# Kernel optimization log

Hardware: AMD Instinct MI355X
Metric: run time of the kernel (lower is better)

Reference implementation:

```python
import jax, jax.numpy as jnp
from jax import lax
import numpy as np

# dims
N_ENT, M, K = 2048, 64, 32              # entities, mentions, candidates per mention
LT, LB, LM, LC, LD = 32, 128, 16, 128, 512  # char lengths: title, body, mention, context, doc
VOCAB, EMB = 5053, 300
H, HH, CCS, W = 256, 128, 512, 5        # hidden, per-dir LSTM hidden, char channels, conv width


def char_cnn(idx, emb, conv_w, conv_b):
    # Conv2d(1, CCS, [EMB, W]) applied to (N,1,EMB,L) == Conv1d(EMB, CCS, W); relu + max-pool over length
    x = jnp.swapaxes(emb[idx], 1, 2)                        # [N, EMB, L]
    y = lax.conv_general_dilated(x, conv_w, (1,), 'VALID')  # [N, CCS, L-W+1]
    return jax.nn.relu(y + conv_b[None, :, None]).max(axis=2)  # [N, CCS]


def _lstm_dir(x, Wih, Whh, bih, bhh):
    pre = x @ Wih.T + (bih + bhh)                            # [B, T, 4*HH]
    def step(carry, g_t):
        h, c = carry
        i, f, g, o = jnp.split(g_t + h @ Whh.T, 4, axis=-1)
        c = jax.nn.sigmoid(f) * c + jax.nn.sigmoid(i) * jnp.tanh(g)
        h = jax.nn.sigmoid(o) * jnp.tanh(c)
        return (h, c), h
    B = x.shape[0]
    z = jnp.zeros((B, Whh.shape[1]), x.dtype)
    _, hs = lax.scan(step, (z, z), jnp.swapaxes(pre, 0, 1))
    return jnp.swapaxes(hs, 0, 1)


def bilstm(x, Wih_f, Whh_f, bih_f, bhh_f, Wih_b, Whh_b, bih_b, bhh_b):
    fwd = _lstm_dir(x, Wih_f, Whh_f, bih_f, bhh_f)
    bwd = _lstm_dir(x[:, ::-1], Wih_b, Whh_b, bih_b, bhh_b)[:, ::-1]
    return jnp.concatenate([fwd, bwd], axis=-1)              # [B, T, H]


def att_flow(c, q, wc, bc, wq, bq, wcq, bcq):
    # BiDAF attention; c,q: [B,T,H] -> [B,T,4H]
    s = (c @ wc)[:, :, None] + (q @ wq)[:, None, :] \
        + jnp.einsum('bid,bjd,d->bij', c, q, wcq) + (bc + bq + bcq)
    a = jax.nn.softmax(s, axis=2)
    c2q = jnp.einsum('bij,bjd->bid', a, q)
    b = jax.nn.softmax(s.max(axis=2), axis=1)
    q2c = jnp.einsum('bi,bid->bd', b, c)[:, None, :]
    return jnp.concatenate([c, c2q, c * c2q, c * jnp.broadcast_to(q2c, c.shape)], axis=-1)


def setup_inputs() -> dict:
    key = jax.random.key(0)
    ks = jax.random.split(key, 16)
    rng = np.random.RandomState(0)
    # exactly K distinct candidate entities per mention (regularized mention_entity indicator)
    cand_idx = jnp.asarray(np.argsort(rng.rand(M, N_ENT), axis=1)[:, :K])
    emb = jax.random.uniform(ks[0], (VOCAB, EMB), jnp.float32, -0.001, 0.001).at[1].set(0.0)
    def rnd(k, shape, s=0.05):
        return jax.random.normal(k, shape, jnp.float32) * s
    return {
        'title_vec': jax.random.randint(ks[1], (N_ENT, LT), 0, VOCAB),
        'body_vec': jax.random.randint(ks[2], (N_ENT, LB), 0, VOCAB),
        'mention_vec': jax.random.randint(ks[3], (M, LM), 0, VOCAB),
        'context_vec': jax.random.randint(ks[4], (M, LC), 0, VOCAB),
        'doc_vec': jax.random.randint(ks[5], (LD,), 0, VOCAB),
        'cand_idx': cand_idx,
        'emb': emb,
        'conv_w': rnd(ks[6], (CCS, EMB, W), 0.02), 'conv_b': jnp.zeros((CCS,), jnp.float32),
        'Wih_f': rnd(ks[7], (4 * HH, CCS)), 'Whh_f': rnd(ks[8], (4 * HH, HH)),
        'bih_f': jnp.zeros((4 * HH,), jnp.float32), 'bhh_f': jnp.zeros((4 * HH,), jnp.float32),
        'Wih_b': rnd(ks[9], (4 * HH, CCS)), 'Whh_b': rnd(ks[10], (4 * HH, HH)),
        'bih_b': jnp.zeros((4 * HH,), jnp.float32), 'bhh_b': jnp.zeros((4 * HH,), jnp.float32),
        'wc': rnd(ks[11], (H,)), 'bc': jnp.zeros((), jnp.float32),
        'wq': rnd(ks[12], (H,)), 'bq': jnp.zeros((), jnp.float32),
        'wcq': rnd(ks[13], (H,)), 'bcq': jnp.zeros((), jnp.float32),
        'wz': rnd(ks[14], (4 * H,)), 'bz': jnp.zeros((), jnp.float32),
        'w_p1': jnp.asarray(0.7, jnp.float32), 'b_p1': jnp.asarray(0.1, jnp.float32),
        'w_p2': jnp.asarray(0.5, jnp.float32), 'b_p2': jnp.asarray(-0.1, jnp.float32),
    }


def reference(title_vec, body_vec, mention_vec, context_vec, doc_vec, cand_idx,
              emb, conv_w, conv_b,
              Wih_f, Whh_f, bih_f, bhh_f, Wih_b, Whh_b, bih_b, bhh_b,
              wc, bc, wq, bq, wcq, bcq, wz, bz, w_p1, b_p1, w_p2, b_p2):
    m, k = cand_idx.shape
    n = title_vec.shape[0]
    lstm_p = (Wih_f, Whh_f, bih_f, bhh_f, Wih_b, Whh_b, bih_b, bhh_b)
    # char-CNN features (compute once per unique sequence, then gather / broadcast)
    title_feat = char_cnn(title_vec, emb, conv_w, conv_b)         # [n, CCS]
    body_feat = char_cnn(body_vec, emb, conv_w, conv_b)           # [n, CCS]
    ctx_feat = char_cnn(context_vec, emb, conv_w, conv_b)         # [m, CCS]
    doc_feat = char_cnn(doc_vec[None], emb, conv_w, conv_b)[0]    # [CCS]
    # per-mention candidate sequences (seq dim = candidates, as in the original loop)
    title_h = bilstm(title_feat[cand_idx], *lstm_p)               # [m, k, H]
    body_h = bilstm(body_feat[cand_idx], *lstm_p)
    ctx_h = bilstm(jnp.broadcast_to(ctx_feat[:, None, :], (m, k, CCS)), *lstm_p)
    doc_h = bilstm(jnp.broadcast_to(doc_feat[None, None, :], (1, k, CCS)), *lstm_p)
    doc_h = jnp.broadcast_to(doc_h, (m, k, H))
    g = att_flow(ctx_h, title_h, wc, bc, wq, bq, wcq, bcq)        # [m, k, 4H]
    h = att_flow(doc_h, body_h, wc, bc, wq, bq, wcq, bcq)
    p1 = g @ wz + bz                                              # [m, k]
    p2 = h @ wz + bz
    score = w_p1 * p1 + b_p1 + w_p2 * p2 + b_p2
    # len(true_output)==1 branch is always taken in the original: raw scores, softmax, sum-normalized
    score_sm = jax.nn.softmax(score, axis=1)
    score_un = score / score.sum(axis=1, keepdims=True)
    rows = jnp.arange(m)[:, None]
    def scatter(v):
        return jnp.zeros((m, n), v.dtype).at[rows, cand_idx].set(v)
    return scatter(score), scatter(score_sm), scatter(score_un)
```

## Files before the change

kernel.cpp:

```cpp
#include <hip/hip_runtime.h>
#include <hip/hip_fp16.h>
#include <math.h>

#define DEDUP_B 34439168ULL
#define AH_B    34459648ULL
#define BH_B    37695488ULL
#define BHP_B   39333888ULL
#define WHH_B   40382464ULL
#define AHP_B   34459648ULL

typedef _Float16 half8 __attribute__((ext_vector_type(8)));
typedef float f32x4 __attribute__((ext_vector_type(4)));

__device__ inline void add8(float* a, float4 r){
  const __half2* h = (const __half2*)&r;
  #pragma unroll
  for (int q = 0; q < 4; ++q){
    float2 f = __half22float2(h[q]);
    a[2*q]   += f.x;
    a[2*q+1] += f.y;
  }
}

__global__ __launch_bounds__(256) void k_init(unsigned int* __restrict__ out32, int n,
                                              unsigned int* __restrict__ dd32,
                                              float* __restrict__ featDoc){
  int t = blockIdx.x * 256 + threadIdx.x;
  if (t < n) out32[t] = 0u;
  if (t < 2112) dd32[t] = 0u;
  if (t < 512) featDoc[t] = 0.f;
}

__global__ __launch_bounds__(256) void k_mark(const int* __restrict__ cand, int* __restrict__ flags){
  int t = blockIdx.x * 256 + threadIdx.x;
  flags[cand[t]] = 1;
}

__global__ __launch_bounds__(256) void k_compact(const int* __restrict__ flags,
                                                 int* __restrict__ nUsed, int* __restrict__ list){
  int t = blockIdx.x * 256 + threadIdx.x;
  if (flags[t]){
    int s = atomicAdd(nUsed, 1);
    list[s] = t;
  }
}

__global__ __launch_bounds__(256) void k_embH(const float* __restrict__ emb, _Float16* __restrict__ A_h){
  int t = blockIdx.x * 256 + threadIdx.x;
  if (t >= 5056 * 320) return;
  int row = t / 320, col = t - row * 320;
  float v = (row < 5053 && col < 300) ? emb[(size_t)row * 300 + col] * 1024.f : 0.f;
  A_h[t] = (_Float16)v;
}

__global__ __launch_bounds__(256) void k_wTh(const float* __restrict__ convw, _Float16* __restrict__ B_h){
  int t = blockIdx.x * 256 + threadIdx.x;
  if (t >= 2560 * 320) return;
  int n = t / 320, k = t - n * 320;
  int w = n >> 9, c = n & 511;
  float v = (k < 300) ? convw[((size_t)c * 300 + k) * 5 + w] : 0.f;
  B_h[t] = (_Float16)v;
}

__global__ __launch_bounds__(256) void k_contrib(const _Float16* __restrict__ A_h,
                                                 const _Float16* __restrict__ B_h,
                                                 __half* __restrict__ contrib){
  int tid = threadIdx.x;
  int lane = tid & 63, wid = tid >> 6;
  int wr = wid >> 1, wc = wid & 1;
  int m0 = blockIdx.x * 64 + wr * 32;
  int n0 = blockIdx.y * 128 + wc * 64;
  int lr = lane & 15, lk = (lane >> 4) * 8;

  const _Float16* Ap = A_h + (size_t)(m0 + lr) * 320 + lk;
  const _Float16* Bp = B_h + (size_t)(n0 + lr) * 320 + lk;

  f32x4 acc[2][4];
  #pragma unroll
  for (int fr = 0; fr < 2; ++fr)
    #pragma unroll
    for (int fc = 0; fc < 4; ++fc) acc[fr][fc] = (f32x4){0.f, 0.f, 0.f, 0.f};

  for (int kk = 0; kk < 320; kk += 32){
    half8 a0 = *(const half8*)(Ap + kk);
    half8 a1 = *(const half8*)(Ap + 16 * 320 + kk);
    half8 b0 = *(const half8*)(Bp + kk);
    half8 b1 = *(const half8*)(Bp + 16 * 320 + kk);
    half8 b2 = *(const half8*)(Bp + 32 * 320 + kk);
    half8 b3 = *(const half8*)(Bp + 48 * 320 + kk);
    acc[0][0] = __builtin_amdgcn_mfma_f32_16x16x32_f16(a0, b0, acc[0][0], 0, 0, 0);
    acc[0][1] = __builtin_amdgcn_mfma_f32_16x16x32_f16(a0, b1, acc[0][1], 0, 0, 0);
    acc[0][2] = __builtin_amdgcn_mfma_f32_16x16x32_f16(a0, b2, acc[0][2], 0, 0, 0);
    acc[0][3] = __builtin_amdgcn_mfma_f32_16x16x32_f16(a0, b3, acc[0][3], 0, 0, 0);
    acc[1][0] = __builtin_amdgcn_mfma_f32_16x16x32_f16(a1, b0, acc[1][0], 0, 0, 0);
    acc[1][1] = __builtin_amdgcn_mfma_f32_16x16x32_f16(a1, b1, acc[1][1], 0, 0, 0);
    acc[1][2] = __builtin_amdgcn_mfma_f32_16x16x32_f16(a1, b2, acc[1][2], 0, 0, 0);
    acc[1][3] = __builtin_amdgcn_mfma_f32_16x16x32_f16(a1, b3, acc[1][3], 0, 0, 0);
  }
  const float s = 1.f / 1024.f;
  #pragma unroll
  for (int fr = 0; fr < 2; ++fr){
    int row = m0 + fr * 16 + (lane >> 4) * 4;
    #pragma unroll
    for (int fc = 0; fc < 4; ++fc){
      int col = n0 + fc * 16 + lr;
      #pragma unroll
      for (int r = 0; r < 4; ++r)
        contrib[(size_t)(row + r) * 2560 + col] = __float2half(acc[fr][fc][r] * s);
    }
  }
}

__global__ __launch_bounds__(256) void k_conv(const int* __restrict__ idx, int L,
                                              const __half* __restrict__ contrib,
                                              const float* __restrict__ convb,
                                              float* __restrict__ featAll, int row0,
                                              const int* __restrict__ list,
                                              const int* __restrict__ nUsed){
  __shared__ int tok[128];
  __shared__ float red[256 * 9];
  int b = blockIdx.x, tid = threadIdx.x;
  int g = b & 7, sIdx = b >> 3;
  int s = sIdx;
  if (list){
    if (sIdx >= *nUsed) return;
    s = list[sIdx];
  }
  const int* row = idx + (size_t)s * L;
  for (int i = tid; i < L; i += 256) tok[i] = row[i];
  __syncthreads();
  int c8 = tid & 7;
  int pg = tid >> 3;
  int cOff = g * 64 + c8 * 8;
  float bias[8], mx[8];
  {
    float4 b0 = *(const float4*)(convb + cOff);
    float4 b1 = *(const float4*)(convb + cOff + 4);
    bias[0]=b0.x; bias[1]=b0.y; bias[2]=b0.z; bias[3]=b0.w;
    bias[4]=b1.x; bias[5]=b1.y; bias[6]=b1.z; bias[7]=b1.w;
  }
  #pragma unroll
  for (int k = 0; k < 8; ++k) mx[k] = 0.f;
  int P = L - 4;
  int per = (P + 31) >> 5;
  int p = pg * per, pe = min(p + per, P);
  for (; p + 1 < pe; p += 2){
    float a0[8], a1[8];
    #pragma unroll
    for (int k = 0; k < 8; ++k){ a0[k] = bias[k]; a1[k] = bias[k]; }
    #pragma unroll
    for (int w = 0; w < 5; ++w){
      float4 r0 = *(const float4*)(contrib + ((size_t)tok[p + w] * 5 + w) * 512 + cOff);
      float4 r1 = *(const float4*)(contrib + ((size_t)tok[p + 1 + w] * 5 + w) * 512 + cOff);
      add8(a0, r0);
      add8(a1, r1);
    }
    #pragma unroll
    for (int k = 0; k < 8; ++k) mx[k] = fmaxf(mx[k], fmaxf(a0[k], a1[k]));
  }
  if (p < pe){
    float a0[8];
    #pragma unroll
    for (int k = 0; k < 8; ++k) a0[k] = bias[k];
    #pragma unroll
    for (int w = 0; w < 5; ++w){
      float4 r0 = *(const float4*)(contrib + ((size_t)tok[p + w] * 5 + w) * 512 + cOff);
      add8(a0, r0);
    }
    #pragma unroll
    for (int k = 0; k < 8; ++k) mx[k] = fmaxf(mx[k], a0[k]);
  }
  #pragma unroll
  for (int k = 0; k < 8; ++k) red[tid * 9 + k] = mx[k];
  __syncthreads();
  if (tid < 64){
    int c8r = tid >> 3, kr = tid & 7;
    float o = red[c8r * 9 + kr];
    #pragma unroll
    for (int q = 1; q < 32; ++q)
      o = fmaxf(o, red[(q * 8 + c8r) * 9 + kr]);
    featAll[(size_t)(row0 + s) * 512 + g * 64 + tid] = o;
  }
}

__global__ __launch_bounds__(256) void k_conv_doc(const int* __restrict__ doc,
                                                  const __half* __restrict__ contrib,
                                                  const float* __restrict__ convb,
                                                  float* __restrict__ featDoc){
  __shared__ int tok[512];
  __shared__ float red[256 * 9];
  int b = blockIdx.x, tid = threadIdx.x;
  for (int i = tid; i < 512; i += 256) tok[i] = doc[i];
  __syncthreads();
  int c8 = tid & 63, pg = tid >> 6;
  float bias[8], mx[8];
  {
    float4 b0 = *(const float4*)(convb + c8 * 8);
    float4 b1 = *(const float4*)(convb + c8 * 8 + 4);
    bias[0]=b0.x; bias[1]=b0.y; bias[2]=b0.z; bias[3]=b0.w;
    bias[4]=b1.x; bias[5]=b1.y; bias[6]=b1.z; bias[7]=b1.w;
  }
  #pragma unroll
  for (int k = 0; k < 8; ++k) mx[k] = 0.f;
  int p0 = b * 16, p1 = min(p0 + 16, 508);
  int n = p1 - p0;
  int per = (n + 3) >> 2;
  int p = p0 + pg * per, pe = min(p + per, p1);
  for (; p < pe; ++p){
    float a0[8];
    #pragma unroll
    for (int k = 0; k < 8; ++k) a0[k] = bias[k];
    #pragma unroll
    for (int w = 0; w < 5; ++w){
      float4 r0 = *(const float4*)(contrib + ((size_t)tok[p + w] * 5 + w) * 512 + c8 * 8);
      add8(a0, r0);
    }
    #pragma unroll
    for (int k = 0; k < 8; ++k) mx[k] = fmaxf(mx[k], a0[k]);
  }
  #pragma unroll
  for (int k = 0; k < 8; ++k) red[tid * 9 + k] = mx[k];
  __syncthreads();
  if (tid < 64){
    #pragma unroll
    for (int k = 0; k < 8; ++k){
      float o = fmaxf(fmaxf(red[tid * 9 + k], red[(tid + 64) * 9 + k]),
                      fmaxf(red[(tid + 128) * 9 + k], red[(tid + 192) * 9 + k]));
      atomicMax((int*)(featDoc + tid * 8 + k), __float_as_int(o));
    }
  }
}

__global__ __launch_bounds__(256) void k_featH(const float* __restrict__ feat, _Float16* __restrict__ A_hp){
  int t = blockIdx.x * 256 + threadIdx.x;
  if (t >= 4224 * 512) return;
  int row = t >> 9;
  float v = (row < 4161) ? feat[t] * 1024.f : 0.f;
  A_hp[t] = (_Float16)v;
}

__global__ __launch_bounds__(256) void k_wihH(const float* __restrict__ Wf,
                                              const float* __restrict__ Wb,
                                              _Float16* __restrict__ B_hp){
  int t = blockIdx.x * 256 + threadIdx.x;
  if (t >= 524288) return;
  int dir = t >> 18, r = t & 262143;
  B_hp[t] = (_Float16)((dir ? Wb : Wf)[r]);
}

__global__ __launch_bounds__(256) void k_whhH(const float* __restrict__ Wf,
                                              const float* __restrict__ Wb,
                                              _Float16* __restrict__ WhhH){
  int t = blockIdx.x * 256 + threadIdx.x;
  if (t >= 131072) return;
  int dir = t >> 16, r = t & 65535;
  WhhH[t] = (_Float16)((dir ? Wb : Wf)[r]);
}

__global__ __launch_bounds__(256) void k_proj(const _Float16* __restrict__ A_hp,
                                              const _Float16* __restrict__ B_hp,
                                              const float* __restrict__ bihF, const float* __restrict__ bhhF,
                                              const float* __restrict__ bihB, const float* __restrict__ bhhB,
                                              float* __restrict__ preAll){
  int tid = threadIdx.x;
  int lane = tid & 63, wid = tid >> 6;
  int wr = wid >> 1, wc = wid & 1;
  int dir = blockIdx.z;
  int m0 = blockIdx.x * 64 + wr * 32;
  int n0 = blockIdx.y * 128 + wc * 64;
  int lr = lane & 15, lk = (lane >> 4) * 8;

  const _Float16* Ap = A_hp + (size_t)(m0 + lr) * 512 + lk;
  const _Float16* Bp = B_hp + (size_t)dir * 262144 + (size_t)(n0 + lr) * 512 + lk;

  f32x4 acc[2][4];
  #pragma unroll
  for (int fr = 0; fr < 2; ++fr)
    #pragma unroll
    for (int fc = 0; fc < 4; ++fc) acc[fr][fc] = (f32x4){0.f, 0.f, 0.f, 0.f};

  for (int kk = 0; kk < 512; kk += 32){
    half8 a0 = *(const half8*)(Ap + kk);
    half8 a1 = *(const half8*)(Ap + 16 * 512 + kk);
    half8 b0 = *(const half8*)(Bp + kk);
    half8 b1 = *(const half8*)(Bp + 16 * 512 + kk);
    half8 b2 = *(const half8*)(Bp + 32 * 512 + kk);
    half8 b3 = *(const half8*)(Bp + 48 * 512 + kk);
    acc[0][0] = __builtin_amdgcn_mfma_f32_16x16x32_f16(a0, b0, acc[0][0], 0, 0, 0);
    acc[0][1] = __builtin_amdgcn_mfma_f32_16x16x32_f16(a0, b1, acc[0][1], 0, 0, 0);
    acc[0][2] = __builtin_amdgcn_mfma_f32_16x16x32_f16(a0, b2, acc[0][2], 0, 0, 0);
    acc[0][3] = __builtin_amdgcn_mfma_f32_16x16x32_f16(a0, b3, acc[0][3], 0, 0, 0);
    acc[1][0] = __builtin_amdgcn_mfma_f32_16x16x32_f16(a1, b0, acc[1][0], 0, 0, 0);
    acc[1][1] = __builtin_amdgcn_mfma_f32_16x16x32_f16(a1, b1, acc[1][1], 0, 0, 0);
    acc[1][2] = __builtin_amdgcn_mfma_f32_16x16x32_f16(a1, b2, acc[1][2], 0, 0, 0);
    acc[1][3] = __builtin_amdgcn_mfma_f32_16x16x32_f16(a1, b3, acc[1][3], 0, 0, 0);
  }
  const float s = 1.f / 1024.f;
  const float* bih = dir ? bihB : bihF;
  const float* bhh = dir ? bhhB : bhhF;
  float* outp = preAll + (size_t)dir * 4176 * 512;
  #pragma unroll
  for (int fr = 0; fr < 2; ++fr){
    int row = m0 + fr * 16 + (lane >> 4) * 4;
    #pragma unroll
    for (int fc = 0; fc < 4; ++fc){
      int col = n0 + fc * 16 + lr;
      float bias = bih[col] + bhh[col];
      #pragma unroll
      for (int r = 0; r < 4; ++r)
        if (row + r < 4176)
          outp[(size_t)(row + r) * 512 + col] = acc[fr][fc][r] * s + bias;
    }
  }
}

__global__ __launch_bounds__(512, 2) void k_recur(const float* __restrict__ preAll,
                                                  const _Float16* __restrict__ WhhH,
                                                  const int* __restrict__ cand,
                                                  float* __restrict__ hT, float* __restrict__ hB,
                                                  float* __restrict__ hC, float* __restrict__ hD){
  int c = blockIdx.x, dir = blockIdx.y, tid = threadIdx.x;
  int lstm = (c < 64) ? 0 : (c < 128) ? 1 : (c < 192) ? 2 : 3;
  int b = (lstm == 3) ? 0 : (c - lstm * 64);
  const float* pre = preAll + (size_t)dir * 4176 * 512;
  float* hout;
  if (lstm == 0)      hout = hT + (size_t)b * 32 * 256;
  else if (lstm == 1) hout = hB + (size_t)b * 32 * 256;
  else if (lstm == 2) hout = hC + (size_t)b * 32 * 256;
  else                hout = hD;
  hout += dir * 128;

  int cidx = tid >> 2;
  int kc = tid & 3;
  int k0 = kc * 32;

  half8 wv[4][4];
  #pragma unroll
  for (int m = 0; m < 4; ++m){
    const _Float16* wp = WhhH + (size_t)dir * 65536 + (size_t)(m * 128 + cidx) * 128 + k0;
    #pragma unroll
    for (int j = 0; j < 4; ++j)
      wv[m][j] = *(const half8*)(wp + j * 8);
  }
  {
    float* wf = (float*)wv;
    #pragma unroll
    for (int i = 0; i < 64; ++i)
      asm volatile("v_mov_b32 %0, %1" : "=v"(wf[i]) : "v"(wf[i]));
  }

  __shared__ __align__(16) float hpad[2][4][36];
  __shared__ int candL[32];
  if (tid < 288) ((float*)hpad)[tid] = 0.f;
  if (lstm < 2 && tid < 32) candL[tid] = cand[b * 32 + tid];
  __syncthreads();

  float pf;
  {
    int t0 = dir ? 31 : 0;
    int rowi;
    if (lstm == 0)      rowi = candL[t0];
    else if (lstm == 1) rowi = 2048 + candL[t0];
    else if (lstm == 2) rowi = 4096 + b;
    else                rowi = 4160;
    pf = pre[(size_t)rowi * 512 + kc * 128 + cidx];
  }

  float cst = 0.f;
  for (int s = 0; s < 32; ++s){
    int t = dir ? (31 - s) : s;
    int cur = s & 1, nxt = cur ^ 1;
    float pfn = 0.f;
    if (s < 31){
      int t2 = dir ? (31 - (s + 1)) : (s + 1);
      int rowi;
      if (lstm == 0)      rowi = candL[t2];
      else if (lstm == 1) rowi = 2048 + candL[t2];
      else if (lstm == 2) rowi = 4096 + b;
      else                rowi = 4160;
      pfn = pre[(size_t)rowi * 512 + kc * 128 + cidx];
    }
    float p0 = 0.f, p1 = 0.f, p2 = 0.f, p3 = 0.f;
    #pragma unroll
    for (int j = 0; j < 4; ++j){
      float4 ha = *(const float4*)&hpad[cur][kc][j * 8];
      float4 hb = *(const float4*)&hpad[cur][kc][j * 8 + 4];
      p0 += (float)wv[0][j][0] * ha.x + (float)wv[0][j][1] * ha.y
          + (float)wv[0][j][2] * ha.z + (float)wv[0][j][3] * ha.w
          + (float)wv[0][j][4] * hb.x + (float)wv[0][j][5] * hb.y
          + (float)wv[0][j][6] * hb.z + (float)wv[0][j][7] * hb.w;
      p1 += (float)wv[1][j][0] * ha.x + (float)wv[1][j][1] * ha.y
          + (float)wv[1][j][2] * ha.z + (float)wv[1][j][3] * ha.w
          + (float)wv[1][j][4] * hb.x + (float)wv[1][j][5] * hb.y
          + (float)wv[1][j][6] * hb.z + (float)wv[1][j][7] * hb.w;
      p2 += (float)wv[2][j][0] * ha.x + (float)wv[2][j][1] * ha.y
          + (float)wv[2][j][2] * ha.z + (float)wv[2][j][3] * ha.w
          + (float)wv[2][j][4] * hb.x + (float)wv[2][j][5] * hb.y
          + (float)wv[2][j][6] * hb.z + (float)wv[2][j][7] * hb.w;
      p3 += (float)wv[3][j][0] * ha.x + (float)wv[3][j][1] * ha.y
          + (float)wv[3][j][2] * ha.z + (float)wv[3][j][3] * ha.w
          + (float)wv[3][j][4] * hb.x + (float)wv[3][j][5] * hb.y
          + (float)wv[3][j][6] * hb.z + (float)wv[3][j][7] * hb.w;
    }
    p0 += __shfl_xor(p0, 1); p0 += __shfl_xor(p0, 2);
    p1 += __shfl_xor(p1, 1); p1 += __shfl_xor(p1, 2);
    p2 += __shfl_xor(p2, 1); p2 += __shfl_xor(p2, 2);
    p3 += __shfl_xor(p3, 1); p3 += __shfl_xor(p3, 2);
    float g = (kc == 0) ? p0 : (kc == 1) ? p1 : (kc == 2) ? p2 : p3;
    g += pf;
    float av = (kc == 2) ? tanhf(g) : 1.f / (1.f + __expf(-g));
    float a1 = __shfl_xor(av, 1);
    float a2 = __shfl_xor(av, 2);
    float a3 = __shfl_xor(av, 3);
    if (kc == 0){
      cst = a1 * cst + av * a2;
      float hf = a3 * tanhf(cst);
      hpad[nxt][cidx >> 5][cidx & 31] = hf;
      hout[(size_t)t * 256 + cidx] = hf;
    }
    pf = pfn;
    __syncthreads();
  }
}

__global__ __launch_bounds__(256) void k_att1(const float* __restrict__ hC,
                                              const float* __restrict__ hT,
                                              const float* __restrict__ hD,
                                              const float* __restrict__ hB,
                                              const float* __restrict__ wc_g, const float* __restrict__ bc_g,
                                              const float* __restrict__ wq_g, const float* __restrict__ bq_g,
                                              const float* __restrict__ wcq_g, const float* __restrict__ bcq_g,
                                              const float* __restrict__ wz_g, const float* __restrict__ bz_g,
                                              double* __restrict__ pOut){
  int b = blockIdx.x, pass = blockIdx.y, tid = threadIdx.x;
  __shared__ float cS[32][260];
  __shared__ float qS[32][260];
  __shared__ float wS[7][256];
  __shared__ double q2cS[256];
  __shared__ double cwS[32], qwS[32], qzS[32], paS[32], smaxS[32], bsmS[32];
  const float* cp = pass ? hD : (hC + (size_t)b * 8192);
  const float* qp = (pass ? hB : hT) + (size_t)b * 8192;
  for (int k = tid; k < 2048; k += 256){
    int i = k >> 6, d4 = (k & 63) * 4;
    *(float4*)&cS[i][d4] = *(const float4*)(cp + i * 256 + d4);
    *(float4*)&qS[i][d4] = *(const float4*)(qp + i * 256 + d4);
  }
  wS[0][tid] = wc_g[tid];
  wS[1][tid] = wq_g[tid];
  wS[2][tid] = wcq_g[tid];
  wS[3][tid] = wz_g[tid];
  wS[4][tid] = wz_g[256 + tid];
  wS[5][tid] = wz_g[512 + tid];
  wS[6][tid] = wz_g[768 + tid];
  __syncthreads();
  int i = tid >> 3, js = tid & 7;
  {
    double a = 0, aq = 0, az = 0;
    for (int k = 0; k < 32; ++k){
      int d = js * 32 + k;
      a  += (double)cS[i][d] * (double)wS[0][d];
      aq += (double)qS[i][d] * (double)wS[1][d];
      az += (double)qS[i][d] * (double)wS[4][d];
    }
    #pragma unroll
    for (int m = 1; m < 8; m <<= 1){
      a  += __shfl_xor(a, m);
      aq += __shfl_xor(aq, m);
      az += __shfl_xor(az, m);
    }
    if (js == 0){ cwS[i] = a; qwS[i] = aq; qzS[i] = az; }
  }
  __syncthreads();
  double bsum = (double)bc_g[0] + (double)bq_g[0] + (double)bcq_g[0];
  double sa[4] = {0,0,0,0}, ta[4] = {0,0,0,0};
  for (int d = 0; d < 256; ++d){
    double cd = (double)cS[i][d];
    double cw1 = cd * (double)wS[2][d];
    double cw2 = cd * (double)wS[5][d];
    #pragma unroll
    for (int m = 0; m < 4; ++m){
      double qv = (double)qS[js + m * 8][d];
      sa[m] += cw1 * qv;
      ta[m] += cw2 * qv;
    }
  }
  {
    double cwv = cwS[i];
    double s[4], mx = -1e300;
    #pragma unroll
    for (int m = 0; m < 4; ++m){
      s[m] = sa[m] + cwv + qwS[js + m * 8] + bsum;
      mx = fmax(mx, s[m]);
    }
    #pragma unroll
    for (int m = 1; m < 8; m <<= 1) mx = fmax(mx, __shfl_xor(mx, m));
    double esum = 0, eacc = 0;
    #pragma unroll
    for (int m = 0; m < 4; ++m){
      double e = exp(s[m] - mx);
      esum += e;
      eacc += e * (qzS[js + m * 8] + ta[m]);
    }
    #pragma unroll
    for (int m = 1; m < 8; m <<= 1){
      esum += __shfl_xor(esum, m);
      eacc += __shfl_xor(eacc, m);
    }
    if (js == 0){ paS[i] = eacc / esum; smaxS[i] = mx; }
  }
  __syncthreads();
  if (tid < 32){
    double v = smaxS[tid];
    double m2 = v;
    #pragma unroll
    for (int m = 1; m < 32; m <<= 1) m2 = fmax(m2, __shfl_xor(m2, m));
    double e = exp(v - m2), ssum = e;
    #pragma unroll
    for (int m = 1; m < 32; m <<= 1) ssum += __shfl_xor(ssum, m);
    bsmS[tid] = e / ssum;
  }
  __syncthreads();
  {
    double a = 0;
    for (int ii = 0; ii < 32; ++ii) a += bsmS[ii] * (double)cS[ii][tid];
    q2cS[tid] = a;
  }
  __syncthreads();
  {
    double t1 = 0, t4 = 0;
    for (int k = 0; k < 32; ++k){
      int d = js * 32 + k;
      double cd = (double)cS[i][d];
      t1 += cd * (double)wS[3][d];
      t4 += cd * q2cS[d] * (double)wS[6][d];
    }
    #pragma unroll
    for (int m = 1; m < 8; m <<= 1){
      t1 += __shfl_xor(t1, m);
      t4 += __shfl_xor(t4, m);
    }
    if (js == 0)
      pOut[((size_t)pass * 64 + b) * 32 + i] = t1 + paS[i] + t4 + (double)bz_g[0];
  }
}

__global__ __launch_bounds__(64) void k_att2(const double* __restrict__ pOut,
                                             const float* __restrict__ wp1_g, const float* __restrict__ bp1_g,
                                             const float* __restrict__ wp2_g, const float* __restrict__ bp2_g,
                                             const int* __restrict__ cand,
                                             float* __restrict__ out){
  int b = blockIdx.x, tid = threadIdx.x;
  if (tid >= 32) return;
  double p1 = pOut[(size_t)b * 32 + tid];
  double p2 = pOut[(size_t)(64 + b) * 32 + tid];
  double sc = (double)wp1_g[0] * p1 + (double)bp1_g[0]
            + (double)wp2_g[0] * p2 + (double)bp2_g[0];
  double mx = sc, rs = sc;
  #pragma unroll
  for (int m = 1; m < 32; m <<= 1){
    mx = fmax(mx, __shfl_xor(mx, m));
    rs += __shfl_xor(rs, m);
  }
  double e = exp(sc - mx), es = e;
  #pragma unroll
  for (int m = 1; m < 32; m <<= 1) es += __shfl_xor(es, m);
  int col = cand[b * 32 + tid];
  out[(size_t)b * 2048 + col] = (float)sc;
  out[131072 + (size_t)b * 2048 + col] = (float)(e / es);
  out[262144 + (size_t)b * 2048 + col] = (float)(sc / rs);
}

extern "C" void kernel_launch(void* const* d_in, const int* in_sizes, int n_in,
                              void* d_out, int out_size, void* d_ws, size_t ws_size,
                              hipStream_t stream) {
  const int* title_v = (const int*)d_in[0];
  const int* body_v  = (const int*)d_in[1];
  const int* ctx_v   = (const int*)d_in[3];
  const int* doc_v   = (const int*)d_in[4];
  const int* cand    = (const int*)d_in[5];
  const float* emb   = (const float*)d_in[6];
  const float* convw = (const float*)d_in[7];
  const float* convb = (const float*)d_in[8];
  const float* WihF  = (const float*)d_in[9];
  const float* WhhF  = (const float*)d_in[10];
  const float* bihF  = (const float*)d_in[11];
  const float* bhhF  = (const float*)d_in[12];
  const float* WihB  = (const float*)d_in[13];
  const float* WhhB  = (const float*)d_in[14];
  const float* bihB  = (const float*)d_in[15];
  const float* bhhB  = (const float*)d_in[16];
  float* out = (float*)d_out;

  const size_t CONTRIB_B = (size_t)5056 * 2560 * 2;
  char* base = (char*)d_ws;
  if (ws_size < 60325888) return;
  __half* contrib = (__half*)base;
  char* featBase = base + CONTRIB_B;
  float* feat = (float*)featBase;
  float* featDoc = feat + (size_t)4160 * 512;

  int* flags = (int*)(base + DEDUP_B);
  int* nUsed = (int*)(base + DEDUP_B + 8192);
  int* list  = (int*)(base + DEDUP_B + 8448);

  _Float16* A_h  = (_Float16*)(base + AH_B);
  _Float16* B_h  = (_Float16*)(base + BH_B);
  _Float16* A_hp = (_Float16*)(base + AHP_B);
  _Float16* B_hp = (_Float16*)(base + BHP_B);
  _Float16* WhhH = (_Float16*)(base + WHH_B);

  float*  preAll = (float*)(base + 2097152);
  float*  hT     = (float*)(base + 19202048);
  float*  hB     = (float*)(base + 21299200);
  float*  hC     = (float*)(base + 23396352);
  float*  hD     = (float*)(base + 25493504);
  double* pOut   = (double*)(base + 25526272);

  k_init<<<(out_size + 255) / 256, 256, 0, stream>>>((unsigned int*)out, out_size,
                                                     (unsigned int*)(base + DEDUP_B), featDoc);
  k_mark<<<8, 256, 0, stream>>>(cand, flags);
  k_compact<<<8, 256, 0, stream>>>(flags, nUsed, list);
  k_embH<<<6320, 256, 0, stream>>>(emb, A_h);
  k_wTh<<<3200, 256, 0, stream>>>(convw, B_h);
  k_contrib<<<dim3(79, 20), 256, 0, stream>>>(A_h, B_h, contrib);

  k_conv<<<16384, 256, 0, stream>>>(title_v, 32, contrib, convb, feat, 0, list, nUsed);
  k_conv<<<16384, 256, 0, stream>>>(body_v, 128, contrib, convb, feat, 2048, list, nUsed);
  k_conv<<<512, 256, 0, stream>>>(ctx_v, 128, contrib, convb, feat, 4096, (const int*)nullptr, (const int*)nullptr);
  k_conv_doc<<<32, 256, 0, stream>>>(doc_v, contrib, convb, featDoc);

  k_featH<<<8448, 256, 0, stream>>>(feat, A_hp);
  k_wihH<<<2048, 256, 0, stream>>>(WihF, WihB, B_hp);
  k_whhH<<<512, 256, 0, stream>>>(WhhF, WhhB, WhhH);
  k_proj<<<dim3(66, 4, 2), 256, 0, stream>>>(A_hp, B_hp, bihF, bhhF, bihB, bhhB, preAll);
  k_recur<<<dim3(193, 2), 512, 0, stream>>>(preAll, WhhH, cand, hT, hB, hC, hD);
  k_att1<<<dim3(64, 2), 256, 0, stream>>>(hC, hT, hD, hB,
                                (const float*)d_in[17], (const float*)d_in[18],
                                (const float*)d_in[19], (const float*)d_in[20],
                                (const float*)d_in[21], (const float*)d_in[22],
                                (const float*)d_in[23], (const float*)d_in[24],
                                pOut);
  k_att2<<<64, 64, 0, stream>>>(pOut,
                                (const float*)d_in[25], (const float*)d_in[26],
                                (const float*)d_in[27], (const float*)d_in[28],
                                cand, out);
}
```

Baseline: 372.5 us.

## Merge prep kernels, batch conv launches, and compute LSTM gates per thread

Folds the zero-init and the four fp16 conversion kernels into one grid-stride prep kernel, and merges the three k_conv launches into a single launch that picks its input from the block index. This removes several kernel launches and the gaps between them. In the LSTM recurrence, every thread now loads all four gate preactivations and computes the cell update itself, replacing the cross-lane shuffles that gathered the gates. This costs redundant transcendental work and more registers in exchange for fewer shuffles on the serial critical path.

```diff
diff --git a/kernel.cpp b/kernel.cpp
--- a/kernel.cpp
+++ b/kernel.cpp
@@ -22,13 +22,50 @@
   }
 }
 
-__global__ __launch_bounds__(256) void k_init(unsigned int* __restrict__ out32, int n,
+__global__ __launch_bounds__(256) void k_prep(unsigned int* __restrict__ out32, int n,
                                               unsigned int* __restrict__ dd32,
-                                              float* __restrict__ featDoc){
-  int t = blockIdx.x * 256 + threadIdx.x;
-  if (t < n) out32[t] = 0u;
-  if (t < 2112) dd32[t] = 0u;
-  if (t < 512) featDoc[t] = 0.f;
+                                              float* __restrict__ featDoc,
+                                              const float* __restrict__ emb, _Float16* __restrict__ A_h,
+                                              const float* __restrict__ convw, _Float16* __restrict__ B_h,
+                                              const float* __restrict__ WihF, const float* __restrict__ WihB,
+                                              _Float16* __restrict__ B_hp,
+                                              const float* __restrict__ WhhF, const float* __restrict__ WhhB,
+                                              _Float16* __restrict__ WhhH){
+  const long o0 = n;
+  const long o1 = o0 + 2112;
+  const long o2 = o1 + 512;
+  const long o3 = o2 + 1617920;
+  const long o4 = o3 + 819200;
+  const long o5 = o4 + 524288;
+  const long o6 = o5 + 131072;
+  for (long t = (long)blockIdx.x * 256 + threadIdx.x; t < o6; t += (long)gridDim.x * 256){
+    if (t < o0){
+      out32[t] = 0u;
+    } else if (t < o1){
+      dd32[t - o0] = 0u;
+    } else if (t < o2){
+      featDoc[t - o1] = 0.f;
+    } else if (t < o3){
+      long u = t - o2;
+      int row = (int)(u / 320), col = (int)(u - (long)row * 320);
+      float v = (row < 5053 && col < 300) ? emb[(size_t)row * 300 + col] * 1024.f : 0.f;
+      A_h[u] = (_Float16)v;
+    } else if (t < o4){
+      long u = t - o3;
+      int nn = (int)(u / 320), k = (int)(u - (long)nn * 320);
+      int w = nn >> 9, c = nn & 511;
+      float v = (k < 300) ? convw[((size_t)c * 300 + k) * 5 + w] : 0.f;
+      B_h[u] = (_Float16)v;
+    } else if (t < o5){
+      long u = t - o4;
+      int dir = (int)(u >> 18), r = (int)(u & 262143);
+      B_hp[u] = (_Float16)((dir ? WihB : WihF)[r]);
+    } else {
+      long u = t - o5;
+      int dir = (int)(u >> 16), r = (int)(u & 65535);
+      WhhH[u] = (_Float16)((dir ? WhhB : WhhF)[r]);
+    }
+  }
 }
 
 __global__ __launch_bounds__(256) void k_mark(const int* __restrict__ cand, int* __restrict__ flags){
@@ -43,23 +80,6 @@
     int s = atomicAdd(nUsed, 1);
     list[s] = t;
   }
-}
-
-__global__ __launch_bounds__(256) void k_embH(const float* __restrict__ emb, _Float16* __restrict__ A_h){
-  int t = blockIdx.x * 256 + threadIdx.x;
-  if (t >= 5056 * 320) return;
-  int row = t / 320, col = t - row * 320;
-  float v = (row < 5053 && col < 300) ? emb[(size_t)row * 300 + col] * 1024.f : 0.f;
-  A_h[t] = (_Float16)v;
-}
-
-__global__ __launch_bounds__(256) void k_wTh(const float* __restrict__ convw, _Float16* __restrict__ B_h){
-  int t = blockIdx.x * 256 + threadIdx.x;
-  if (t >= 2560 * 320) return;
-  int n = t / 320, k = t - n * 320;
-  int w = n >> 9, c = n & 511;
-  float v = (k < 300) ? convw[((size_t)c * 300 + k) * 5 + w] : 0.f;
-  B_h[t] = (_Float16)v;
 }
 
 __global__ __launch_bounds__(256) void k_contrib(const _Float16* __restrict__ A_h,
@@ -111,18 +131,24 @@
   }
 }
 
-__global__ __launch_bounds__(256) void k_conv(const int* __restrict__ idx, int L,
+__global__ __launch_bounds__(256) void k_conv(const int* __restrict__ title_v,
+                                              const int* __restrict__ body_v,
+                                              const int* __restrict__ ctx_v,
                                               const __half* __restrict__ contrib,
                                               const float* __restrict__ convb,
-                                              float* __restrict__ featAll, int row0,
+                                              float* __restrict__ featAll,
                                               const int* __restrict__ list,
                                               const int* __restrict__ nUsed){
   __shared__ int tok[128];
   __shared__ float red[256 * 9];
-  int b = blockIdx.x, tid = threadIdx.x;
-  int g = b & 7, sIdx = b >> 3;
+  int bg = blockIdx.x, tid = threadIdx.x;
+  const int* idx; int L, row0; bool useList;
+  if (bg < 16384){ idx = title_v; L = 32;  row0 = 0;    useList = true; }
+  else if (bg < 32768){ bg -= 16384; idx = body_v; L = 128; row0 = 2048; useList = true; }
+  else { bg -= 32768; idx = ctx_v; L = 128; row0 = 4096; useList = false; }
+  int g = bg & 7, sIdx = bg >> 3;
   int s = sIdx;
-  if (list){
+  if (useList){
     if (sIdx >= *nUsed) return;
     s = list[sIdx];
   }
@@ -237,24 +263,6 @@
   int row = t >> 9;
   float v = (row < 4161) ? feat[t] * 1024.f : 0.f;
   A_hp[t] = (_Float16)v;
-}
-
-__global__ __launch_bounds__(256) void k_wihH(const float* __restrict__ Wf,
-                                              const float* __restrict__ Wb,
-                                              _Float16* __restrict__ B_hp){
-  int t = blockIdx.x * 256 + threadIdx.x;
-  if (t >= 524288) return;
-  int dir = t >> 18, r = t & 262143;
-  B_hp[t] = (_Float16)((dir ? Wb : Wf)[r]);
-}
-
-__global__ __launch_bounds__(256) void k_whhH(const float* __restrict__ Wf,
-                                              const float* __restrict__ Wb,
-                                              _Float16* __restrict__ WhhH){
-  int t = blockIdx.x * 256 + threadIdx.x;
-  if (t >= 131072) return;
-  int dir = t >> 16, r = t & 65535;
-  WhhH[t] = (_Float16)((dir ? Wb : Wf)[r]);
 }
 
 __global__ __launch_bounds__(256) void k_proj(const _Float16* __restrict__ A_hp,
@@ -355,7 +363,7 @@
   if (lstm < 2 && tid < 32) candL[tid] = cand[b * 32 + tid];
   __syncthreads();
 
-  float pf;
+  float pf0, pf1, pf2, pf3;
   {
     int t0 = dir ? 31 : 0;
     int rowi;
@@ -363,14 +371,15 @@
     else if (lstm == 1) rowi = 2048 + candL[t0];
     else if (lstm == 2) rowi = 4096 + b;
     else                rowi = 4160;
-    pf = pre[(size_t)rowi * 512 + kc * 128 + cidx];
+    const float* pr = pre + (size_t)rowi * 512 + cidx;
+    pf0 = pr[0]; pf1 = pr[128]; pf2 = pr[256]; pf3 = pr[384];
   }
 
   float cst = 0.f;
   for (int s = 0; s < 32; ++s){
     int t = dir ? (31 - s) : s;
     int cur = s & 1, nxt = cur ^ 1;
-    float pfn = 0.f;
+    float pn0 = 0.f, pn1 = 0.f, pn2 = 0.f, pn3 = 0.f;
     if (s < 31){
       int t2 = dir ? (31 - (s + 1)) : (s + 1);
       int rowi;
@@ -378,7 +387,8 @@
       else if (lstm == 1) rowi = 2048 + candL[t2];
       else if (lstm == 2) rowi = 4096 + b;
       else                rowi = 4160;
-      pfn = pre[(size_t)rowi * 512 + kc * 128 + cidx];
+      const float* pr = pre + (size_t)rowi * 512 + cidx;
+      pn0 = pr[0]; pn1 = pr[128]; pn2 = pr[256]; pn3 = pr[384];
     }
     float p0 = 0.f, p1 = 0.f, p2 = 0.f, p3 = 0.f;
     #pragma unroll
@@ -406,19 +416,17 @@
     p1 += __shfl_xor(p1, 1); p1 += __shfl_xor(p1, 2);
     p2 += __shfl_xor(p2, 1); p2 += __shfl_xor(p2, 2);
     p3 += __shfl_xor(p3, 1); p3 += __shfl_xor(p3, 2);
-    float g = (kc == 0) ? p0 : (kc == 1) ? p1 : (kc == 2) ? p2 : p3;
-    g += pf;
-    float av = (kc == 2) ? tanhf(g) : 1.f / (1.f + __expf(-g));
-    float a1 = __shfl_xor(av, 1);
-    float a2 = __shfl_xor(av, 2);
-    float a3 = __shfl_xor(av, 3);
+    float si = 1.f / (1.f + __expf(-(p0 + pf0)));
+    float sf = 1.f / (1.f + __expf(-(p1 + pf1)));
+    float tg = tanhf(p2 + pf2);
+    float so = 1.f / (1.f + __expf(-(p3 + pf3)));
+    cst = sf * cst + si * tg;
+    float hf = so * tanhf(cst);
     if (kc == 0){
-      cst = a1 * cst + av * a2;
-      float hf = a3 * tanhf(cst);
       hpad[nxt][cidx >> 5][cidx & 31] = hf;
       hout[(size_t)t * 256 + cidx] = hf;
     }
-    pf = pfn;
+    pf0 = pn0; pf1 = pn1; pf2 = pn2; pf3 = pn3;
     __syncthreads();
   }
 }
@@ -616,22 +624,18 @@
   float*  hD     = (float*)(base + 25493504);
   double* pOut   = (double*)(base + 25526272);
 
-  k_init<<<(out_size + 255) / 256, 256, 0, stream>>>((unsigned int*)out, out_size,
-                                                     (unsigned int*)(base + DEDUP_B), featDoc);
+  k_prep<<<4096, 256, 0, stream>>>((unsigned int*)out, out_size,
+                                   (unsigned int*)(base + DEDUP_B), featDoc,
+                                   emb, A_h, convw, B_h, WihF, WihB, B_hp,
+                                   WhhF, WhhB, WhhH);
   k_mark<<<8, 256, 0, stream>>>(cand, flags);
   k_compact<<<8, 256, 0, stream>>>(flags, nUsed, list);
-  k_embH<<<6320, 256, 0, stream>>>(emb, A_h);
-  k_wTh<<<3200, 256, 0, stream>>>(convw, B_h);
   k_contrib<<<dim3(79, 20), 256, 0, stream>>>(A_h, B_h, contrib);
 
-  k_conv<<<16384, 256, 0, stream>>>(title_v, 32, contrib, convb, feat, 0, list, nUsed);
-  k_conv<<<16384, 256, 0, stream>>>(body_v, 128, contrib, convb, feat, 2048, list, nUsed);
-  k_conv<<<512, 256, 0, stream>>>(ctx_v, 128, contrib, convb, feat, 4096, (const int*)nullptr, (const int*)nullptr);
+  k_conv<<<33280, 256, 0, stream>>>(title_v, body_v, ctx_v, contrib, convb, feat, list, nUsed);
   k_conv_doc<<<32, 256, 0, stream>>>(doc_v, contrib, convb, featDoc);
 
   k_featH<<<8448, 256, 0, stream>>>(feat, A_hp);
-  k_wihH<<<2048, 256, 0, stream>>>(WihF, WihB, B_hp);
-  k_whhH<<<512, 256, 0, stream>>>(WhhF, WhhB, WhhH);
   k_proj<<<dim3(66, 4, 2), 256, 0, stream>>>(A_hp, B_hp, bihF, bhhF, bihB, bhhB, preAll);
   k_recur<<<dim3(193, 2), 512, 0, stream>>>(preAll, WhhH, cand, hT, hB, hC, hD);
   k_att1<<<dim3(64, 2), 256, 0, stream>>>(hC, hT, hD, hB,
```

Result: no change. 378.9 us (+1.7%).
